# Optimization experiments

Measured on AMD Instinct MI355X. Metric: run time of the kernel, lower is better.

The kernel has to match this reference:

```python
import jax, jax.numpy as jnp
import numpy as np

TEMPERATURE = 0.5  # init temperature; attn_drop=0.0 so dropout is identity


def setup_inputs() -> dict:
    key = jax.random.key(0)
    k1, k2, k3 = jax.random.split(key, 3)
    B, H, N, D = 4, 8, 2048, 64
    q = jax.random.normal(k1, (B, H, N, D), dtype=jnp.float32)
    k = jax.random.normal(k2, (B, H, N, D), dtype=jnp.float32)
    v = jax.random.normal(k3, (B, H, N, D), dtype=jnp.float32)
    scale = jnp.asarray(D ** -0.5, dtype=jnp.float32)
    return {"q": q, "k": k, "v": v, "scale": scale}


def reference(q, k, v, scale):
    # logits: [B,H,N,N]
    logits = jnp.einsum("bhqd,bhkd->bhqk", q, k) * scale
    # first softmax acts as a soft mask over keys
    soft_mask = jax.nn.softmax(logits / TEMPERATURE, axis=-1)
    # second softmax over masked logits (elementwise product, NOT matmul)
    attn = jax.nn.softmax(logits * soft_mask, axis=-1)
    # dropout with p=0.0 is identity
    out = jnp.einsum("bhqk,bhkd->bhqd", attn, v)
    return out
```

## Files before the change

kernel.cpp:

```cpp
#include <hip/hip_runtime.h>


typedef _Float16 f16;
typedef f16 f16x8 __attribute__((ext_vector_type(8)));
typedef f16 f16x4 __attribute__((ext_vector_type(4)));
typedef float f32x4 __attribute__((ext_vector_type(4)));

#define MFMA32(a, b, c) __builtin_amdgcn_mfma_f32_16x16x32_f16((a), (b), (c), 0, 0, 0)
#define MFMA16(a, b, c) __builtin_amdgcn_mfma_f32_16x16x16f16((a), (b), (c), 0, 0, 0)
#define EXP2(x) __builtin_amdgcn_exp2f(x)

#define N_CTX 2048
#define DH 64
#define KT 64
#define NKT_G 16
#define ROWS 128
#define QS 72
#define KSB (KT * QS)
#define SMEM_BYTES (4 * 2 * KSB * 2 + 2048)

#define C2 2.885390081777927f

__device__ inline unsigned pk(float a, float b) {
    typedef __fp16 fp16x2_t __attribute__((ext_vector_type(2)));
    union { fp16x2_t v; unsigned u; } x;
    x.v = __builtin_amdgcn_cvt_pkrtz(a, b);
    return x.u;
}

__global__ __launch_bounds__(256)
void stk_prep(const float* __restrict__ kg, const float* __restrict__ vg,
              f16* __restrict__ wsK, f16* __restrict__ wsV) {
    const int bid = blockIdx.x, tid = threadIdx.x;
    if (bid < 2048) {
        int g = bid * 256 + tid;
        int bh = g >> 14, key = (g >> 3) & 2047, c = g & 7;
        const float* src = kg + (((size_t)bh * 2048 + key) << 6) + c * 8;
        float4 a = *(const float4*)src;
        float4 b = *(const float4*)(src + 4);
        uint4 o;
        o.x = pk(a.x, a.y); o.y = pk(a.z, a.w);
        o.z = pk(b.x, b.y); o.w = pk(b.z, b.w);
        *(uint4*)&wsK[(((size_t)bh * 2048 + key) << 6) + c * 8] = o;
    } else {
        int g = (bid - 2048) * 256 + tid;
        int d = g & 63, c2 = (g >> 6) & 7, t = (g >> 9) & 31, bh = g >> 14;
        const float* vbase = vg + (((size_t)bh * 2048 + t * 64) << 6) + d;
        float vals[8];
        #pragma unroll
        for (int j = 0; j < 8; ++j) {
            int c = c2 * 8 + j;
            int key = ((c >> 2) & 3) * 16 + ((c >> 4) & 3) * 4 + (c & 3);
            vals[j] = vbase[key << 6];
        }
        uint4 o;
        o.x = pk(vals[0], vals[1]); o.y = pk(vals[2], vals[3]);
        o.z = pk(vals[4], vals[5]); o.w = pk(vals[6], vals[7]);
        *(uint4*)&wsV[((((size_t)bh * 32 + t) << 6) + d) * 64 + c2 * 8] = o;
    }
}

__global__ __launch_bounds__(1024, 8)
void stk_attn_mfma(const float* __restrict__ qg, const f16* __restrict__ wsK,
                   const f16* __restrict__ wsV, const float* __restrict__ sg,
                   float* __restrict__ og) {
    extern __shared__ f16 smem[];

    const int tid  = threadIdx.x;
    const int wv   = tid >> 6;
    const int grp  = wv >> 3;
    const int wv7  = wv & 7;
    const int lane = tid & 63;
    const int l15  = lane & 15;
    const int q4   = lane >> 4;
    const int tg   = (wv7 << 6) | lane;
    const int bh   = blockIdx.x & 31;
    const int q0   = (blockIdx.x >> 5) * ROWS;
    const float scale2 = sg[0] * C2;

    const float* qb = qg + (size_t)bh * N_CTX * DH;
    float*       ob = og + (size_t)bh * N_CTX * DH;
    const f16* wsKh = wsK + ((size_t)bh << 17);
    const f16* wsVh = wsV + ((size_t)bh << 17);
    const int T0 = grp * NKT_G;

    f16x8 aq[2];
    {
        const float* qrow = qb + (size_t)(q0 + wv7 * 16 + l15) * DH;
        #pragma unroll
        for (int kc = 0; kc < 2; ++kc) {
            float4 a0 = *(const float4*)&qrow[kc * 32 + q4 * 8];
            float4 a1 = *(const float4*)&qrow[kc * 32 + q4 * 8 + 4];
            union { f16x8 h; unsigned u[4]; } A;
            A.u[0] = pk(a0.x * scale2, a0.y * scale2);
            A.u[1] = pk(a0.z * scale2, a0.w * scale2);
            A.u[2] = pk(a1.x * scale2, a1.y * scale2);
            A.u[3] = pk(a1.z * scale2, a1.w * scale2);
            aq[kc] = A.h;
        }
    }

    f16* const ksBase = smem + grp * (2 * KSB);
    f16* const vtBase = smem + 2 * (2 * KSB) + grp * (2 * KSB);
    float* const sred = (float*)(smem + 4 * (2 * KSB));
    float* const obuf = (float*)smem;

    const int sofs = tg * 8;
    const int wofs = (tg >> 3) * QS + (tg & 7) * 8;

    f16* const ks_w = ksBase;
    const f16* const ks_r = ksBase + l15 * QS + q4 * 8;
    f16* const vt_w = vtBase;
    const f16* const vt_r = vtBase + l15 * QS + q4 * 16;

    float s1 = 0.f;
    f16x8 krh;
    krh = *(const f16x8*)&wsKh[(size_t)T0 * 4096 + sofs];
    *(f16x8*)&ks_w[wofs] = krh;
    krh = *(const f16x8*)&wsKh[(size_t)(T0 + 1) * 4096 + sofs];
    __syncthreads();

    for (int kt = 0; kt < NKT_G; ++kt) {
        const int cur = (kt & 1) * KSB, nxt = KSB - cur;
        *(f16x8*)&ks_w[nxt + wofs] = krh;
        { int tn = (kt + 2 < NKT_G) ? kt + 2 : NKT_G - 1;
          krh = *(const f16x8*)&wsKh[(size_t)(T0 + tn) * 4096 + sofs]; }
        __builtin_amdgcn_s_setprio(1);
        #pragma unroll
        for (int kgi = 0; kgi < 4; ++kgi) {
            f16x8 b0 = *(const f16x8*)&ks_r[cur + kgi * 16 * QS];
            f16x8 b1 = *(const f16x8*)&ks_r[cur + kgi * 16 * QS + 32];
            f32x4 acc = {0.f, 0.f, 0.f, 0.f};
            acc = MFMA32(b0, aq[0], acc);
            acc = MFMA32(b1, aq[1], acc);
            s1 += (EXP2(acc[0]) + EXP2(acc[1])) + (EXP2(acc[2]) + EXP2(acc[3]));
        }
        __builtin_amdgcn_s_setprio(0);
        __syncthreads();
    }
    s1 += __shfl_xor(s1, 16, 64);
    s1 += __shfl_xor(s1, 32, 64);
    if (lane < 16) sred[(grp << 7) + (wv7 << 4) + lane] = s1;
    __syncthreads();
    s1 += sred[((grp ^ 1) << 7) + (wv7 << 4) + l15];
    const float inv1 = 0.5f / s1;

    f32x4 O[4];
    #pragma unroll
    for (int dt = 0; dt < 4; ++dt) O[dt] = (f32x4){0.f, 0.f, 0.f, 0.f};
    f32x4 Oe = {0.f, 0.f, 0.f, 0.f};
    const f16x4 ones = {(f16)1.f, (f16)1.f, (f16)1.f, (f16)1.f};

    f16x8 vrh;
    krh = *(const f16x8*)&wsKh[(size_t)T0 * 4096 + sofs];
    vrh = *(const f16x8*)&wsVh[(size_t)T0 * 4096 + sofs];
    *(f16x8*)&ks_w[wofs] = krh;
    *(f16x8*)&vt_w[wofs] = vrh;
    krh = *(const f16x8*)&wsKh[(size_t)(T0 + 1) * 4096 + sofs];
    vrh = *(const f16x8*)&wsVh[(size_t)(T0 + 1) * 4096 + sofs];
    __syncthreads();

    for (int kt = 0; kt < NKT_G; ++kt) {
        const int cur = (kt & 1) * KSB, nxt = KSB - cur;
        *(f16x8*)&ks_w[nxt + wofs] = krh;
        *(f16x8*)&vt_w[nxt + wofs] = vrh;
        { int tn = (kt + 2 < NKT_G) ? kt + 2 : NKT_G - 1;
          krh = *(const f16x8*)&wsKh[(size_t)(T0 + tn) * 4096 + sofs];
          vrh = *(const f16x8*)&wsVh[(size_t)(T0 + tn) * 4096 + sofs]; }
        __builtin_amdgcn_s_setprio(1);
        #pragma unroll
        for (int p = 0; p < 2; ++p) {
            f16x4 pfr[2];
            #pragma unroll
            for (int h = 0; h < 2; ++h) {
                const int kgi = p * 2 + h;
                f16x8 b0 = *(const f16x8*)&ks_r[cur + kgi * 16 * QS];
                f16x8 b1 = *(const f16x8*)&ks_r[cur + kgi * 16 * QS + 32];
                f32x4 acc = {0.f, 0.f, 0.f, 0.f};
                acc = MFMA32(b0, aq[0], acc);
                acc = MFMA32(b1, aq[1], acc);
                float e2r[4];
                #pragma unroll
                for (int r = 0; r < 4; ++r) {
                    float a  = acc[r];
                    float e1 = EXP2(a);
                    e2r[r] = EXP2((a * e1) * inv1);
                }
                union { f16x4 hh; unsigned u[2]; } P;
                P.u[0] = pk(e2r[0], e2r[1]);
                P.u[1] = pk(e2r[2], e2r[3]);
                pfr[h] = P.hh;
                Oe = MFMA16(ones, pfr[h], Oe);
            }
            #pragma unroll
            for (int dt = 0; dt < 4; ++dt) {
                f16x8 av = *(const f16x8*)&vt_r[cur + dt * 16 * QS + p * 8];
                f16x4 alo = __builtin_shufflevector(av, av, 0, 1, 2, 3);
                f16x4 ahi = __builtin_shufflevector(av, av, 4, 5, 6, 7);
                O[dt] = MFMA16(alo, pfr[0], O[dt]);
                O[dt] = MFMA16(ahi, pfr[1], O[dt]);
            }
        }
        __builtin_amdgcn_s_setprio(0);
        __syncthreads();
    }

    const int rec = tg * 20;
    if (grp) {
        #pragma unroll
        for (int dt = 0; dt < 4; ++dt)
            *(f32x4*)&obuf[rec + dt * 4] = O[dt];
        obuf[rec + 16] = Oe[0];
    }
    __syncthreads();
    if (!grp) {
        #pragma unroll
        for (int dt = 0; dt < 4; ++dt)
            O[dt] += *(const f32x4*)&obuf[rec + dt * 4];
        const float invl2 = 1.0f / (Oe[0] + obuf[rec + 16]);
        const size_t orow = (size_t)(q0 + wv7 * 16 + l15) * DH;
        #pragma unroll
        for (int dt = 0; dt < 4; ++dt) {
            float4 o;
            o.x = O[dt][0] * invl2;
            o.y = O[dt][1] * invl2;
            o.z = O[dt][2] * invl2;
            o.w = O[dt][3] * invl2;
            *(float4*)&ob[orow + dt * 16 + q4 * 4] = o;
        }
    }
}

extern "C" void kernel_launch(void* const* d_in, const int* in_sizes, int n_in,
                              void* d_out, int out_size, void* d_ws, size_t ws_size,
                              hipStream_t stream) {
    const float* q = (const float*)d_in[0];
    const float* k = (const float*)d_in[1];
    const float* v = (const float*)d_in[2];
    const float* s = (const float*)d_in[3];
    float* out = (float*)d_out;
    f16* wsK = (f16*)d_ws;
    f16* wsV = wsK + (size_t)32 * N_CTX * DH;
    stk_prep<<<dim3(4096), dim3(256), 0, stream>>>(k, v, wsK, wsV);
    dim3 grid(32 * 16);
    stk_attn_mfma<<<grid, 1024, SMEM_BYTES, stream>>>(q, wsK, wsV, s, out);
}
```

Baseline: 171.9 us.

## Transpose V through LDS in prep and double K tile per pass-1 stage

The V-prep branch now reads coalesced float4 rows, transposes and packs them to fp16 through a shared-memory tile, and writes 16-element vectors. This replaces strided scalar gathers and cuts the V-prep grid from 2048 to 1024 blocks. The first (softmax-denominator) pass now stages two K tiles per iteration, using the idle V buffer as the second ping-pong slot. That halves the number of barriers in that pass at the cost of more registers for prefetch. A barrier is added before the second pass reuses the buffers.

```diff
diff --git a/kernel.cpp b/kernel.cpp
--- a/kernel.cpp
+++ b/kernel.cpp
@@ -43,20 +43,30 @@
         o.z = pk(b.x, b.y); o.w = pk(b.z, b.w);
         *(uint4*)&wsK[(((size_t)bh * 2048 + key) << 6) + c * 8] = o;
     } else {
-        int g = (bid - 2048) * 256 + tid;
-        int d = g & 63, c2 = (g >> 6) & 7, t = (g >> 9) & 31, bh = g >> 14;
-        const float* vbase = vg + (((size_t)bh * 2048 + t * 64) << 6) + d;
-        float vals[8];
-        #pragma unroll
-        for (int j = 0; j < 8; ++j) {
-            int c = c2 * 8 + j;
-            int key = ((c >> 2) & 3) * 16 + ((c >> 4) & 3) * 4 + (c & 3);
-            vals[j] = vbase[key << 6];
-        }
-        uint4 o;
-        o.x = pk(vals[0], vals[1]); o.y = pk(vals[2], vals[3]);
-        o.z = pk(vals[4], vals[5]); o.w = pk(vals[6], vals[7]);
-        *(uint4*)&wsV[((((size_t)bh * 32 + t) << 6) + d) * 64 + c2 * 8] = o;
+        __shared__ f16 lds[DH * QS];
+        const int bid2 = bid - 2048;
+        const int bh = bid2 >> 5, t = bid2 & 31;
+        const int p = tid >> 3, dseg = tid & 7, d0 = dseg * 8;
+        const int c0 = ((p >> 1) & 3) * 16 + ((p >> 3) & 3) * 4 + (p & 1) * 2;
+        const float* base = vg + (((size_t)(bh * 2048 + t * 64 + 2 * p)) << 6) + d0;
+        float4 a0 = *(const float4*)(base);
+        float4 a1 = *(const float4*)(base + 4);
+        float4 b0 = *(const float4*)(base + 64);
+        float4 b1 = *(const float4*)(base + 68);
+        #pragma unroll
+        for (int j = 0; j < 4; ++j) {
+            *(unsigned*)&lds[(d0 + j) * QS + c0] =
+                pk(((const float*)&a0)[j], ((const float*)&b0)[j]);
+            *(unsigned*)&lds[(d0 + 4 + j) * QS + c0] =
+                pk(((const float*)&a1)[j], ((const float*)&b1)[j]);
+        }
+        __syncthreads();
+        const int d = tid >> 2, cs = tid & 3;
+        f16x8 r0 = *(const f16x8*)&lds[d * QS + cs * 16];
+        f16x8 r1 = *(const f16x8*)&lds[d * QS + cs * 16 + 8];
+        f16* dst = wsV + ((((size_t)bh * 32 + t) << 6) + d) * 64 + cs * 16;
+        *(f16x8*)(dst) = r0;
+        *(f16x8*)(dst + 8) = r1;
     }
 }
 
@@ -108,28 +118,35 @@
     const int sofs = tg * 8;
     const int wofs = (tg >> 3) * QS + (tg & 7) * 8;
 
-    f16* const ks_w = ksBase;
     const f16* const ks_r = ksBase + l15 * QS + q4 * 8;
-    f16* const vt_w = vtBase;
+    const f16* const ksrB = vtBase + l15 * QS + q4 * 8;
     const f16* const vt_r = vtBase + l15 * QS + q4 * 16;
 
     float s1 = 0.f;
-    f16x8 krh;
-    krh = *(const f16x8*)&wsKh[(size_t)T0 * 4096 + sofs];
-    *(f16x8*)&ks_w[wofs] = krh;
-    krh = *(const f16x8*)&wsKh[(size_t)(T0 + 1) * 4096 + sofs];
-    __syncthreads();
-
-    for (int kt = 0; kt < NKT_G; ++kt) {
-        const int cur = (kt & 1) * KSB, nxt = KSB - cur;
-        *(f16x8*)&ks_w[nxt + wofs] = krh;
-        { int tn = (kt + 2 < NKT_G) ? kt + 2 : NKT_G - 1;
-          krh = *(const f16x8*)&wsKh[(size_t)(T0 + tn) * 4096 + sofs]; }
+    f16x8 kr2[2];
+    kr2[0] = *(const f16x8*)&wsKh[(size_t)T0 * 4096 + sofs];
+    kr2[1] = *(const f16x8*)&wsKh[(size_t)(T0 + 1) * 4096 + sofs];
+    *(f16x8*)&ksBase[wofs] = kr2[0];
+    *(f16x8*)&ksBase[KSB + wofs] = kr2[1];
+    kr2[0] = *(const f16x8*)&wsKh[(size_t)(T0 + 2) * 4096 + sofs];
+    kr2[1] = *(const f16x8*)&wsKh[(size_t)(T0 + 3) * 4096 + sofs];
+    __syncthreads();
+
+    for (int st = 0; st < 8; ++st) {
+        f16* const nxtb = (st & 1) ? ksBase : vtBase;
+        const f16* const crd = (st & 1) ? ksrB : ks_r;
+        *(f16x8*)&nxtb[wofs] = kr2[0];
+        *(f16x8*)&nxtb[KSB + wofs] = kr2[1];
+        {
+            int tn = (st + 2 < 8) ? st + 2 : 7;
+            kr2[0] = *(const f16x8*)&wsKh[(size_t)(T0 + 2 * tn) * 4096 + sofs];
+            kr2[1] = *(const f16x8*)&wsKh[(size_t)(T0 + 2 * tn + 1) * 4096 + sofs];
+        }
         __builtin_amdgcn_s_setprio(1);
         #pragma unroll
-        for (int kgi = 0; kgi < 4; ++kgi) {
-            f16x8 b0 = *(const f16x8*)&ks_r[cur + kgi * 16 * QS];
-            f16x8 b1 = *(const f16x8*)&ks_r[cur + kgi * 16 * QS + 32];
+        for (int kgi = 0; kgi < 8; ++kgi) {
+            f16x8 b0 = *(const f16x8*)&crd[kgi * 16 * QS];
+            f16x8 b1 = *(const f16x8*)&crd[kgi * 16 * QS + 32];
             f32x4 acc = {0.f, 0.f, 0.f, 0.f};
             acc = MFMA32(b0, aq[0], acc);
             acc = MFMA32(b1, aq[1], acc);
@@ -151,9 +168,12 @@
     f32x4 Oe = {0.f, 0.f, 0.f, 0.f};
     const f16x4 ones = {(f16)1.f, (f16)1.f, (f16)1.f, (f16)1.f};
 
-    f16x8 vrh;
+    f16* const ks_w = ksBase;
+    f16* const vt_w = vtBase;
+    f16x8 krh, vrh;
     krh = *(const f16x8*)&wsKh[(size_t)T0 * 4096 + sofs];
     vrh = *(const f16x8*)&wsVh[(size_t)T0 * 4096 + sofs];
+    __syncthreads();
     *(f16x8*)&ks_w[wofs] = krh;
     *(f16x8*)&vt_w[wofs] = vrh;
     krh = *(const f16x8*)&wsKh[(size_t)(T0 + 1) * 4096 + sofs];
@@ -241,7 +261,7 @@
     float* out = (float*)d_out;
     f16* wsK = (f16*)d_ws;
     f16* wsV = wsK + (size_t)32 * N_CTX * DH;
-    stk_prep<<<dim3(4096), dim3(256), 0, stream>>>(k, v, wsK, wsV);
+    stk_prep<<<dim3(3072), dim3(256), 0, stream>>>(k, v, wsK, wsV);
     dim3 grid(32 * 16);
     stk_attn_mfma<<<grid, 1024, SMEM_BYTES, stream>>>(q, wsK, wsV, s, out);
 }
```

New measurement: 170.3 us. Within noise of the previous version (-0.9%).
